# Kernel optimization log

Measured on AMD Instinct MI355X. Metric: run time of the kernel, lower is better.

The kernel has to match this reference:

```python
import jax, jax.numpy as jnp
import numpy as np

B, S, E, H = 4, 1024, 256, 8
D = E // H


def setup_inputs() -> dict:
    key = jax.random.key(0)
    ks = jax.random.split(key, 10)
    def lin(k, fin, fout):
        return jax.random.normal(k, (fin, fout), jnp.float32) / np.sqrt(fin)
    return {
        'x': jax.random.normal(ks[0], (B, S, E), jnp.float32),
        'Wq': lin(ks[1], E, E),
        'Wk': lin(ks[2], E, E),
        'Wv': lin(ks[3], E, E),
        'W_off1': lin(ks[4], E, E // 2),
        'b_off1': jnp.zeros((E // 2,), jnp.float32),
        'W_off2': lin(ks[5], E // 2, 2 * H),
        'b_off2': jnp.zeros((2 * H,), jnp.float32),
        'W_out': lin(ks[6], E, E),
        'b_out': jnp.zeros((E,), jnp.float32),
    }


def _forward(x, Wq, Wk, Wv, W_off1, b_off1, W_off2, b_off2, W_out, b_out):
    Bb, Ss, Ee = x.shape
    scale = 1.0 / np.sqrt(D)
    # offsets: (B,S,H,2) -- [...,0]=x-offset (col), [...,1]=y-offset (row)
    off = jax.nn.gelu(x @ W_off1 + b_off1, approximate=False) @ W_off2 + b_off2
    off = off.reshape(Bb, Ss, H, 2)
    q = (x @ Wq).reshape(Bb, Ss, H, D).transpose(0, 2, 1, 3)  # bhsd
    k = (x @ Wk).reshape(Bb, Ss, H, D).transpose(0, 2, 1, 3)
    v = (x @ Wv).reshape(Bb, Ss, H, D).transpose(0, 2, 1, 3)
    scores = jnp.einsum('bhid,bhjd->bhij', q, k) * scale  # (B,H,S,S)

    ox = off[..., 0].transpose(0, 2, 1)  # (B,H,S)
    oy = off[..., 1].transpose(0, 2, 1)
    cols = jnp.arange(Ss, dtype=x.dtype)
    xs = cols[None, None, None, :] + ox[..., None]          # (B,H,S,S) sample col
    ys = cols[None, None, :, None] + oy[..., None]          # (B,H,S,1) sample row

    x0 = jnp.floor(xs); x1 = x0 + 1.0
    y0 = jnp.floor(ys); y1 = y0 + 1.0
    wx = xs - x0  # (B,H,S,S)
    wy = ys - y0  # (B,H,S,1)
    lim = jnp.asarray(Ss - 1, x.dtype)

    def corner(yf, xf):
        # bilinear corner sample with zeros padding (align_corners=True)
        yc = jnp.clip(yf, 0, lim).astype(jnp.int32)
        xc = jnp.clip(xf, 0, lim).astype(jnp.int32)
        rows = jnp.take_along_axis(scores, jnp.broadcast_to(yc, scores.shape), axis=2)
        vals = jnp.take_along_axis(rows, jnp.broadcast_to(xc, rows.shape), axis=3)
        valid = (yf >= 0) & (yf <= lim) & (xf >= 0) & (xf <= lim)
        return jnp.where(valid, vals, jnp.zeros((), x.dtype))

    deformed = (corner(y0, x0) * (1 - wy) * (1 - wx)
                + corner(y0, x1) * (1 - wy) * wx
                + corner(y1, x0) * wy * (1 - wx)
                + corner(y1, x1) * wy * wx)

    attn = jax.nn.softmax(deformed, axis=-1)  # dropout is identity in eval
    out = jnp.einsum('bhij,bhjd->bhid', attn, v)
    out = out.transpose(0, 2, 1, 3).reshape(Bb, Ss, Ee)
    return out @ W_out + b_out


def reference(x, Wq, Wk, Wv, W_off1, b_off1, W_off2, b_off2, W_out, b_out):
    return _forward(x, Wq, Wk, Wv, W_off1, b_off1, W_off2, b_off2, W_out, b_out)
```

## Files before the change

kernel.cpp:

```cpp
#include <hip/hip_runtime.h>

typedef unsigned short u16;
typedef __attribute__((ext_vector_type(8))) unsigned short ushort8_t;
typedef __attribute__((ext_vector_type(8))) short short8;
typedef __attribute__((ext_vector_type(4))) float f32x4;

__device__ __forceinline__ float bf2f(u16 u) {
    union { unsigned int i; float f; } z;
    z.i = ((unsigned int)u) << 16;
    return z.f;
}
__device__ __forceinline__ u16 f2bf(float f) {
    union { float f; unsigned int i; } z;
    z.f = f;
    unsigned int i = z.i;
    return (u16)((i + 0x7fffu + ((i >> 16) & 1u)) >> 16);
}
__device__ __forceinline__ int sniff_bf16(const u16* __restrict__ x) {
    u16 u = x[threadIdx.x & 63];
    int e = (u >> 7) & 0xFF;
    bool sane = (e >= 110 && e <= 135) || (u == 0);
    unsigned long long m = __ballot(sane);
    return (__popcll(m) >= 50) ? 1 : 0;
}
__device__ __forceinline__ float cvt_elem(const void* p, int i, int fl) {
    return fl ? bf2f(((const u16*)p)[i]) : ((const float*)p)[i];
}

#define SB 1024
#define EB 256
#define NH 8
#define HD 32

__global__ __launch_bounds__(256) void k_convx(
    const void* x, const void* w2, const void* b1, const void* b2, const void* bo,
    u16* __restrict__ xb, u16* __restrict__ W2t, float* __restrict__ b1f,
    float* __restrict__ b2f, float* __restrict__ bof) {
    int fl = sniff_bf16((const u16*)x);
    int t = threadIdx.x;
    if (blockIdx.x < 1024) {
        int idx = blockIdx.x * 1024 + t * 4;
        if (fl) {
            *(ushort4*)(xb + idx) = *(const ushort4*)((const u16*)x + idx);
        } else {
            float4 v = *(const float4*)((const float*)x + idx);
            ushort4 s;
            s.x = f2bf(v.x); s.y = f2bf(v.y); s.z = f2bf(v.z); s.w = f2bf(v.w);
            *(ushort4*)(xb + idx) = s;
        }
    } else {
        #pragma unroll
        for (int it = 0; it < 10; ++it) {
            int idx = it * 256 + t;
            if (idx < 2048) {
                int n = idx >> 7, kk = idx & 127;
                W2t[idx] = f2bf(cvt_elem(w2, kk * 16 + n, fl));
            }
            else if (idx < 2176)  b1f[idx - 2048] = cvt_elem(b1, idx - 2048, fl);
            else if (idx < 2192)  b2f[idx - 2176] = cvt_elem(b2, idx - 2176, fl);
            else if (idx < 2448)  bof[idx - 2192] = cvt_elem(bo, idx - 2192, fl);
        }
    }
}

__global__ __launch_bounds__(256) void k_trans(
    const void* wq, const void* wk, const void* wv, const void* w1, const void* wo,
    const u16* __restrict__ xsniff, u16* __restrict__ Wcat, u16* __restrict__ Wot) {
    __shared__ float tile[64][65];
    int fl = sniff_bf16(xsniff);
    int z = blockIdx.z;
    const void* src;
    u16* dst;
    int ncols;
    if (z == 0)      { src = wq; dst = Wcat;             ncols = 256; }
    else if (z == 1) { src = wk; dst = Wcat + 256 * 256; ncols = 256; }
    else if (z == 2) { src = wv; dst = Wcat + 512 * 256; ncols = 256; }
    else if (z == 3) { src = w1; dst = Wcat + 768 * 256; ncols = 128; }
    else             { src = wo; dst = Wot;              ncols = 256; }
    int k0 = blockIdx.x * 64, n0 = blockIdx.y * 64;
    if (n0 >= ncols) return;
    int t = threadIdx.x;
    int lr = t >> 6, lc = t & 63;
    #pragma unroll
    for (int it = 0; it < 16; ++it) {
        int r = it * 4 + lr;
        tile[r][lc] = cvt_elem(src, (k0 + r) * ncols + n0 + lc, fl);
    }
    __syncthreads();
    #pragma unroll
    for (int it = 0; it < 16; ++it) {
        int n = it * 4 + lr;
        dst[(size_t)(n0 + n) * 256 + k0 + lc] = f2bf(tile[lc][n]);
    }
}

__global__ __launch_bounds__(256) void k_qkvh(
    const u16* __restrict__ xb, const u16* __restrict__ Wt, const float* __restrict__ b1f,
    u16* __restrict__ q, u16* __restrict__ k, u16* __restrict__ v, u16* __restrict__ hb) {
    int t = threadIdx.x;
    int w = t >> 6, L = t & 63;
    int lane15 = L & 15, quad = L >> 4;
    int Wid = blockIdx.x * 4 + w;
    int mtile = Wid & 127, ntile = Wid >> 7;
    int m0 = mtile * 32, n0 = ntile * 32;
    const u16* ap0 = xb + (size_t)(m0 + lane15) * 256 + quad * 8;
    const u16* ap1 = ap0 + 16 * 256;
    const u16* bp0 = Wt + (size_t)(n0 + lane15) * 256 + quad * 8;
    const u16* bp1 = bp0 + 16 * 256;
    f32x4 acc[2][2];
    #pragma unroll
    for (int a = 0; a < 2; ++a)
        #pragma unroll
        for (int c = 0; c < 2; ++c) acc[a][c] = (f32x4){0.0f, 0.0f, 0.0f, 0.0f};
    #pragma unroll
    for (int kc = 0; kc < 256; kc += 32) {
        short8 a0 = *(const short8*)(ap0 + kc);
        short8 a1 = *(const short8*)(ap1 + kc);
        short8 b0 = *(const short8*)(bp0 + kc);
        short8 b1 = *(const short8*)(bp1 + kc);
        acc[0][0] = __builtin_amdgcn_mfma_f32_16x16x32_bf16(a0, b0, acc[0][0], 0, 0, 0);
        acc[0][1] = __builtin_amdgcn_mfma_f32_16x16x32_bf16(a0, b1, acc[0][1], 0, 0, 0);
        acc[1][0] = __builtin_amdgcn_mfma_f32_16x16x32_bf16(a1, b0, acc[1][0], 0, 0, 0);
        acc[1][1] = __builtin_amdgcn_mfma_f32_16x16x32_bf16(a1, b1, acc[1][1], 0, 0, 0);
    }
    if (ntile < 16) {
        u16* dst = (ntile < 8) ? q : k;
        int nl = (ntile & 7) * 32;
        #pragma unroll
        for (int mt = 0; mt < 2; ++mt)
            #pragma unroll
            for (int nt = 0; nt < 2; ++nt)
                #pragma unroll
                for (int reg = 0; reg < 4; ++reg) {
                    int m = m0 + mt * 16 + quad * 4 + reg;
                    int n = nl + nt * 16 + lane15;
                    int b = m >> 10, s = m & 1023, hh = n >> 5, d = n & 31;
                    dst[(((size_t)(b * NH + hh)) * SB + s) * HD + d] = f2bf(acc[mt][nt][reg]);
                }
    } else if (ntile < 24) {
        int nl = (ntile - 16) * 32;
        #pragma unroll
        for (int mt = 0; mt < 2; ++mt)
            #pragma unroll
            for (int nt = 0; nt < 2; ++nt)
                #pragma unroll
                for (int reg = 0; reg < 4; ++reg) {
                    int m = m0 + mt * 16 + quad * 4 + reg;
                    int n = nl + nt * 16 + lane15;
                    int b = m >> 10, s = m & 1023, hh = n >> 5, d = n & 31;
                    v[(b * NH + hh) * (SB * HD) + (s >> 3) * 256 + d * 8 + (s & 7)] =
                        f2bf(acc[mt][nt][reg]);
                }
    } else {
        int nl = (ntile - 24) * 32;
        #pragma unroll
        for (int mt = 0; mt < 2; ++mt)
            #pragma unroll
            for (int nt = 0; nt < 2; ++nt)
                #pragma unroll
                for (int reg = 0; reg < 4; ++reg) {
                    int m = m0 + mt * 16 + quad * 4 + reg;
                    int hn = nl + nt * 16 + lane15;
                    float aa = acc[mt][nt][reg] + b1f[hn];
                    float g = 0.5f * aa * (1.0f + erff(aa * 0.70710678118654752f));
                    hb[(size_t)m * 128 + hn] = f2bf(g);
                }
    }
}

__global__ __launch_bounds__(256) void k_qprime(
    const u16* __restrict__ hb, const u16* __restrict__ W2t, const float* __restrict__ b2f,
    float2* __restrict__ prmA, float4* __restrict__ prmB) {
    int t = threadIdx.x;
    int w = t >> 6, L = t & 63;
    int lane15 = L & 15, quad = L >> 4;
    int m0 = (blockIdx.x * 4 + w) * 16;
    const u16* ap = hb + (size_t)(m0 + lane15) * 128 + quad * 8;
    const u16* bp = W2t + (size_t)lane15 * 128 + quad * 8;
    f32x4 acc = {0.0f, 0.0f, 0.0f, 0.0f};
    #pragma unroll
    for (int c = 0; c < 4; ++c) {
        short8 a = *(const short8*)(ap + c * 32);
        short8 bfr = *(const short8*)(bp + c * 32);
        acc = __builtin_amdgcn_mfma_f32_16x16x32_bf16(a, bfr, acc, 0, 0, 0);
    }
    const float scale = 0.17677669529663687f;
    int n = lane15, h = n >> 1;
    float bb = b2f[n];
    #pragma unroll
    for (int reg = 0; reg < 4; ++reg) {
        int m = m0 + quad * 4 + reg;
        int i = m & 1023;
        float val = acc[reg] + bb;
        if ((n & 1) == 0) {
            float fxf = floorf(val);
            float wx = val - fxf;
            fxf = fminf(fmaxf(fxf, -1028.0f), 1028.0f);
            prmA[m * 8 + h] = make_float2(fxf, wx);
        } else {
            float ysf = (float)i + val;
            float y0f = floorf(ysf);
            float wy = ysf - y0f;
            float y1f = y0f + 1.0f;
            float alA = scale * (1.0f - wy) * ((y0f >= 0.0f && y0f <= 1023.0f) ? 1.0f : 0.0f);
            float alB = scale * wy * ((y1f >= 0.0f && y1f <= 1023.0f) ? 1.0f : 0.0f);
            float yc0 = fminf(fmaxf(y0f, 0.0f), 1023.0f);
            float yc1 = fminf(fmaxf(y1f, 0.0f), 1023.0f);
            prmB[m * 8 + h] = make_float4(alA, alB, yc0, yc1);
        }
    }
}

#define TSTR 1064
#define BLEND4A(R)                                                    \
    _Pragma("unroll")                                                 \
    for (int jj = 0; jj < 4; ++jj) {                                  \
        float dd = wxm * A8[(R) + jj] + wx * A8[(R) + jj + 1];        \
        dv[c * 4 + jj] = dd;                                          \
        lmax = fmaxf(lmax, dd);                                       \
    }

__global__ __launch_bounds__(256) void k_attn(
    const u16* __restrict__ q, const u16* __restrict__ kmat,
    const float2* __restrict__ prmA, const float4* __restrict__ prmB,
    const u16* __restrict__ vfrag, u16* __restrict__ attn) {
    __shared__ u16 tbuf[16][TSTR];
    __shared__ float invLs[16];
    float* red = (float*)&tbuf[0][0];
    int t = threadIdx.x;
    int w = t >> 6, L = t & 63;
    int lane15 = L & 15, quad = L >> 4;
    int bh = blockIdx.y, it0 = blockIdx.x * 16;
    int b = bh >> 3, h = bh & 7;
    int mg0 = b * SB + it0;

    const u16* qb = q + (size_t)bh * SB * HD;
    float4 pB = prmB[(size_t)(mg0 + lane15) * 8 + h];
    int yc0 = (int)pB.z, yc1 = (int)pB.w;
    short8 q0 = *(const short8*)(qb + yc0 * HD + quad * 8);
    short8 q1 = *(const short8*)(qb + yc1 * HD + quad * 8);
    union { short8 v; u16 a[8]; } afr;
    #pragma unroll
    for (int s = 0; s < 8; ++s)
        afr.a[s] = f2bf(pB.x * bf2f((u16)q0[s]) + pB.y * bf2f((u16)q1[s]));

    const u16* kb = kmat + (size_t)bh * SB * HD;
    int c0 = w * 256;
    #pragma unroll
    for (int nt = 0; nt < 16; ++nt) {
        short8 bk = *(const short8*)(kb + (size_t)(c0 + nt * 16 + lane15) * HD + quad * 8);
        f32x4 z = {0.0f, 0.0f, 0.0f, 0.0f};
        f32x4 acc = __builtin_amdgcn_mfma_f32_16x16x32_bf16(afr.v, bk, z, 0, 0, 0);
        #pragma unroll
        for (int reg = 0; reg < 4; ++reg)
            tbuf[quad * 4 + reg][16 + c0 + nt * 16 + lane15] = f2bf(acc[reg]);
    }
    __syncthreads();

    #pragma unroll
    for (int r = 0; r < 4; ++r) {
        int m = w * 4 + r;
        float2 pA = prmA[(size_t)(mg0 + m) * 8 + h];
        int fx = (int)pA.x;
        float wx = pA.y, wxm = 1.0f - wx;
        int qd = fx >> 2, rm = fx & 3;
        float dv[16];
        float lmax = -3.0e38f;
        #pragma unroll
        for (int c = 0; c < 4; ++c) {
            int colbase = c * 256 + 4 * (qd + L);
            int rd = colbase < -16 ? -16 : (colbase > 1032 ? 1032 : colbase);
            const u16* rp = &tbuf[m][16 + rd];
            ushort4 lo = *(const ushort4*)rp;
            ushort4 hi = *(const ushort4*)(rp + 4);
            u16 av[8] = {lo.x, lo.y, lo.z, lo.w, hi.x, hi.y, hi.z, hi.w};
            float A8[8];
            #pragma unroll
            for (int s = 0; s < 8; ++s) {
                bool ok = (unsigned)(colbase + s) < 1024u;
                A8[s] = ok ? bf2f(av[s]) : 0.0f;
            }
            if (rm == 0) { BLEND4A(0) }
            else if (rm == 1) { BLEND4A(1) }
            else if (rm == 2) { BLEND4A(2) }
            else { BLEND4A(3) }
        }
        #pragma unroll
        for (int o = 1; o < 64; o <<= 1) lmax = fmaxf(lmax, __shfl_xor(lmax, o));
        float ls = 0.0f;
        #pragma unroll
        for (int z = 0; z < 16; ++z) { dv[z] = __expf(dv[z] - lmax); ls += dv[z]; }
        #pragma unroll
        for (int o = 1; o < 64; o <<= 1) ls += __shfl_xor(ls, o);
        #pragma unroll
        for (int c = 0; c < 4; ++c) {
            unsigned lo = (unsigned)f2bf(dv[c * 4 + 0]) | ((unsigned)f2bf(dv[c * 4 + 1]) << 16);
            unsigned hi = (unsigned)f2bf(dv[c * 4 + 2]) | ((unsigned)f2bf(dv[c * 4 + 3]) << 16);
            *(uint2*)&tbuf[m][16 + c * 256 + 4 * L] = make_uint2(lo, hi);
        }
        if (L == 0) invLs[m] = 1.0f / ls;
    }
    __syncthreads();

    const u16* vb = vfrag + bh * (SB * HD);
    f32x4 acc0 = {0.0f, 0.0f, 0.0f, 0.0f};
    f32x4 acc1 = {0.0f, 0.0f, 0.0f, 0.0f};
    int kc0 = w * 256;
    #pragma unroll
    for (int c = 0; c < 8; ++c) {
        int kc = kc0 + c * 32;
        short8 a = *(const short8*)&tbuf[lane15][16 + kc + quad * 8];
        const u16* bp = vb + ((kc >> 3) + quad) * (HD * 8);
        short8 b0 = *(const short8*)(bp + lane15 * 8);
        short8 b1 = *(const short8*)(bp + (lane15 + 16) * 8);
        acc0 = __builtin_amdgcn_mfma_f32_16x16x32_bf16(a, b0, acc0, 0, 0, 0);
        acc1 = __builtin_amdgcn_mfma_f32_16x16x32_bf16(a, b1, acc1, 0, 0, 0);
    }
    __syncthreads();
    *(f32x4*)&red[(((size_t)w * 2 + 0) * 64 + L) * 4] = acc0;
    *(f32x4*)&red[(((size_t)w * 2 + 1) * 64 + L) * 4] = acc1;
    __syncthreads();
    {
        int row = t >> 4, col = t & 15;
        int lsrc = col + 16 * (row >> 2);
        int reg = row & 3;
        float s0 = red[((0 * 64 + lsrc)) * 4 + reg] + red[((2 * 64 + lsrc)) * 4 + reg]
                 + red[((4 * 64 + lsrc)) * 4 + reg] + red[((6 * 64 + lsrc)) * 4 + reg];
        float s1 = red[((1 * 64 + lsrc)) * 4 + reg] + red[((3 * 64 + lsrc)) * 4 + reg]
                 + red[((5 * 64 + lsrc)) * 4 + reg] + red[((7 * 64 + lsrc)) * 4 + reg];
        float il = invLs[row];
        size_t o = ((size_t)(b * SB + it0 + row)) * EB + h * HD;
        attn[o + col]      = f2bf(s0 * il);
        attn[o + 16 + col] = f2bf(s1 * il);
    }
}

__global__ __launch_bounds__(256) void k_out(
    const u16* __restrict__ a, const u16* __restrict__ Wot, const float* __restrict__ bof,
    const u16* __restrict__ xsniff, void* __restrict__ outp) {
    int fl = sniff_bf16(xsniff);
    int t = threadIdx.x;
    int w = t >> 6, L = t & 63;
    int lane15 = L & 15, quad = L >> 4;
    int Wid = blockIdx.x * 4 + w;
    int m0 = (Wid & 255) * 16, n0 = (Wid >> 8) * 32;
    const u16* ap  = a + (size_t)(m0 + lane15) * 256 + quad * 8;
    const u16* bp0 = Wot + (size_t)(n0 + lane15) * 256 + quad * 8;
    const u16* bp1 = bp0 + 16 * 256;
    f32x4 acc0 = {0.0f, 0.0f, 0.0f, 0.0f};
    f32x4 acc1 = {0.0f, 0.0f, 0.0f, 0.0f};
    #pragma unroll
    for (int kc = 0; kc < 256; kc += 32) {
        short8 av = *(const short8*)(ap + kc);
        short8 b0 = *(const short8*)(bp0 + kc);
        short8 b1 = *(const short8*)(bp1 + kc);
        acc0 = __builtin_amdgcn_mfma_f32_16x16x32_bf16(av, b0, acc0, 0, 0, 0);
        acc1 = __builtin_amdgcn_mfma_f32_16x16x32_bf16(av, b1, acc1, 0, 0, 0);
    }
    #pragma unroll
    for (int nt = 0; nt < 2; ++nt) {
        const f32x4& ac = nt ? acc1 : acc0;
        #pragma unroll
        for (int reg = 0; reg < 4; ++reg) {
            int m = m0 + quad * 4 + reg;
            int n = n0 + nt * 16 + lane15;
            float val = ac[reg] + bof[n];
            if (fl) ((u16*)outp)[(size_t)m * 256 + n] = f2bf(val);
            else    ((float*)outp)[(size_t)m * 256 + n] = val;
        }
    }
}

extern "C" void kernel_launch(void* const* d_in, const int* in_sizes, int n_in,
                              void* d_out, int out_size, void* d_ws, size_t ws_size,
                              hipStream_t stream) {
    char* ws = (char*)d_ws;
    u16*    xb   = (u16*)(ws);
    u16*    Wcat = (u16*)(ws + 2097152);
    u16*    Wot  = (u16*)(ws + 2555904);
    u16*    W2t  = (u16*)(ws + 2686976);
    float*  b1f  = (float*)(ws + 2691072);
    float*  b2f  = (float*)(ws + 2691584);
    float*  bof  = (float*)(ws + 2691648);
    u16*    q    = (u16*)(ws + 2692672);
    u16*    k    = (u16*)(ws + 4789824);
    u16*    v    = (u16*)(ws + 6886976);
    u16*    hb   = (u16*)(ws + 8984128);
    u16*    attn = (u16*)(ws + 10032704);
    float2* prmA = (float2*)(ws + 12129856);
    float4* prmB = (float4*)(ws + 12392000);

    hipLaunchKernelGGL(k_convx, dim3(1025), dim3(256), 0, stream,
                       d_in[0], d_in[6], d_in[5], d_in[7], d_in[9],
                       xb, W2t, b1f, b2f, bof);
    hipLaunchKernelGGL(k_trans, dim3(4, 4, 5), dim3(256), 0, stream,
                       d_in[1], d_in[2], d_in[3], d_in[4], d_in[8],
                       (const u16*)d_in[0], Wcat, Wot);
    hipLaunchKernelGGL(k_qkvh, dim3(896), dim3(256), 0, stream, xb, Wcat, b1f, q, k, v, hb);
    hipLaunchKernelGGL(k_qprime, dim3(64), dim3(256), 0, stream, hb, W2t, b2f, prmA, prmB);
    hipLaunchKernelGGL(k_attn, dim3(64, 32), dim3(256), 0, stream, q, k, prmA, prmB, v, attn);
    hipLaunchKernelGGL(k_out, dim3(512), dim3(256), 0, stream, attn, Wot, bof,
                       (const u16*)d_in[0], (u16*)d_out);
}
```

Before: 149.9 us.

## Merge prep kernels, swap MFMA operands for vectorized stores, zero-pad score tile

Merges the input-conversion and weight-transpose kernels into one launch, which removes a kernel launch. Swaps the MFMA A/B operands in the QKV, attention-score and output GEMMs so each lane holds four contiguous output columns and can issue packed 64-bit or float4 stores instead of scalar ones. Zero-fills the padding columns of the shared score tile, so the per-element bounds masks in the bilinear blend can be dropped, and shrinks the row stride. The stride change may bring back LDS bank conflicts, and correctness now depends on the padding being wide enough.

```diff
diff --git a/kernel.cpp b/kernel.cpp
--- a/kernel.cpp
+++ b/kernel.cpp
@@ -1,7 +1,6 @@
 #include <hip/hip_runtime.h>
 
 typedef unsigned short u16;
-typedef __attribute__((ext_vector_type(8))) unsigned short ushort8_t;
 typedef __attribute__((ext_vector_type(8))) short short8;
 typedef __attribute__((ext_vector_type(4))) float f32x4;
 
@@ -32,14 +31,18 @@
 #define NH 8
 #define HD 32
 
-__global__ __launch_bounds__(256) void k_convx(
-    const void* x, const void* w2, const void* b1, const void* b2, const void* bo,
-    u16* __restrict__ xb, u16* __restrict__ W2t, float* __restrict__ b1f,
-    float* __restrict__ b2f, float* __restrict__ bof) {
+__global__ __launch_bounds__(256) void k_prep(
+    const void* x, const void* wq, const void* wk, const void* wv, const void* w1,
+    const void* w2, const void* wo, const void* b1, const void* b2, const void* bo,
+    u16* __restrict__ xb, u16* __restrict__ Wcat, u16* __restrict__ Wot,
+    u16* __restrict__ W2t, float* __restrict__ b1f, float* __restrict__ b2f,
+    float* __restrict__ bof) {
+    __shared__ float tile[64][65];
     int fl = sniff_bf16((const u16*)x);
     int t = threadIdx.x;
-    if (blockIdx.x < 1024) {
-        int idx = blockIdx.x * 1024 + t * 4;
+    int bid = blockIdx.x;
+    if (bid < 1024) {
+        int idx = bid * 1024 + t * 4;
         if (fl) {
             *(ushort4*)(xb + idx) = *(const ushort4*)((const u16*)x + idx);
         } else {
@@ -48,7 +51,7 @@
             s.x = f2bf(v.x); s.y = f2bf(v.y); s.z = f2bf(v.z); s.w = f2bf(v.w);
             *(ushort4*)(xb + idx) = s;
         }
-    } else {
+    } else if (bid == 1024) {
         #pragma unroll
         for (int it = 0; it < 10; ++it) {
             int idx = it * 256 + t;
@@ -60,37 +63,31 @@
             else if (idx < 2192)  b2f[idx - 2176] = cvt_elem(b2, idx - 2176, fl);
             else if (idx < 2448)  bof[idx - 2192] = cvt_elem(bo, idx - 2192, fl);
         }
-    }
-}
-
-__global__ __launch_bounds__(256) void k_trans(
-    const void* wq, const void* wk, const void* wv, const void* w1, const void* wo,
-    const u16* __restrict__ xsniff, u16* __restrict__ Wcat, u16* __restrict__ Wot) {
-    __shared__ float tile[64][65];
-    int fl = sniff_bf16(xsniff);
-    int z = blockIdx.z;
-    const void* src;
-    u16* dst;
-    int ncols;
-    if (z == 0)      { src = wq; dst = Wcat;             ncols = 256; }
-    else if (z == 1) { src = wk; dst = Wcat + 256 * 256; ncols = 256; }
-    else if (z == 2) { src = wv; dst = Wcat + 512 * 256; ncols = 256; }
-    else if (z == 3) { src = w1; dst = Wcat + 768 * 256; ncols = 128; }
-    else             { src = wo; dst = Wot;              ncols = 256; }
-    int k0 = blockIdx.x * 64, n0 = blockIdx.y * 64;
-    if (n0 >= ncols) return;
-    int t = threadIdx.x;
-    int lr = t >> 6, lc = t & 63;
-    #pragma unroll
-    for (int it = 0; it < 16; ++it) {
-        int r = it * 4 + lr;
-        tile[r][lc] = cvt_elem(src, (k0 + r) * ncols + n0 + lc, fl);
-    }
-    __syncthreads();
-    #pragma unroll
-    for (int it = 0; it < 16; ++it) {
-        int n = it * 4 + lr;
-        dst[(size_t)(n0 + n) * 256 + k0 + lc] = f2bf(tile[lc][n]);
+    } else {
+        int rel = bid - 1025;
+        int z = rel >> 4, rr = rel & 15;
+        int k0 = (rr & 3) * 64, n0 = (rr >> 2) * 64;
+        const void* src;
+        u16* dst;
+        int ncols;
+        if (z == 0)      { src = wq; dst = Wcat;             ncols = 256; }
+        else if (z == 1) { src = wk; dst = Wcat + 256 * 256; ncols = 256; }
+        else if (z == 2) { src = wv; dst = Wcat + 512 * 256; ncols = 256; }
+        else if (z == 3) { src = w1; dst = Wcat + 768 * 256; ncols = 128; }
+        else             { src = wo; dst = Wot;              ncols = 256; }
+        if (n0 >= ncols) return;
+        int lr = t >> 6, lc = t & 63;
+        #pragma unroll
+        for (int it = 0; it < 16; ++it) {
+            int r = it * 4 + lr;
+            tile[r][lc] = cvt_elem(src, (k0 + r) * ncols + n0 + lc, fl);
+        }
+        __syncthreads();
+        #pragma unroll
+        for (int it = 0; it < 16; ++it) {
+            int n = it * 4 + lr;
+            dst[(size_t)(n0 + n) * 256 + k0 + lc] = f2bf(tile[lc][n]);
+        }
     }
 }
 
@@ -107,64 +104,84 @@
     const u16* ap1 = ap0 + 16 * 256;
     const u16* bp0 = Wt + (size_t)(n0 + lane15) * 256 + quad * 8;
     const u16* bp1 = bp0 + 16 * 256;
+    bool vreg = (ntile >= 16 && ntile < 24);
     f32x4 acc[2][2];
     #pragma unroll
     for (int a = 0; a < 2; ++a)
         #pragma unroll
         for (int c = 0; c < 2; ++c) acc[a][c] = (f32x4){0.0f, 0.0f, 0.0f, 0.0f};
-    #pragma unroll
-    for (int kc = 0; kc < 256; kc += 32) {
-        short8 a0 = *(const short8*)(ap0 + kc);
-        short8 a1 = *(const short8*)(ap1 + kc);
-        short8 b0 = *(const short8*)(bp0 + kc);
-        short8 b1 = *(const short8*)(bp1 + kc);
-        acc[0][0] = __builtin_amdgcn_mfma_f32_16x16x32_bf16(a0, b0, acc[0][0], 0, 0, 0);
-        acc[0][1] = __builtin_amdgcn_mfma_f32_16x16x32_bf16(a0, b1, acc[0][1], 0, 0, 0);
-        acc[1][0] = __builtin_amdgcn_mfma_f32_16x16x32_bf16(a1, b0, acc[1][0], 0, 0, 0);
-        acc[1][1] = __builtin_amdgcn_mfma_f32_16x16x32_bf16(a1, b1, acc[1][1], 0, 0, 0);
+    if (!vreg) {
+        #pragma unroll
+        for (int kc = 0; kc < 256; kc += 32) {
+            short8 a0 = *(const short8*)(ap0 + kc);
+            short8 a1 = *(const short8*)(ap1 + kc);
+            short8 b0 = *(const short8*)(bp0 + kc);
+            short8 b1 = *(const short8*)(bp1 + kc);
+            acc[0][0] = __builtin_amdgcn_mfma_f32_16x16x32_bf16(b0, a0, acc[0][0], 0, 0, 0);
+            acc[0][1] = __builtin_amdgcn_mfma_f32_16x16x32_bf16(b1, a0, acc[0][1], 0, 0, 0);
+            acc[1][0] = __builtin_amdgcn_mfma_f32_16x16x32_bf16(b0, a1, acc[1][0], 0, 0, 0);
+            acc[1][1] = __builtin_amdgcn_mfma_f32_16x16x32_bf16(b1, a1, acc[1][1], 0, 0, 0);
+        }
+    } else {
+        #pragma unroll
+        for (int kc = 0; kc < 256; kc += 32) {
+            short8 a0 = *(const short8*)(ap0 + kc);
+            short8 a1 = *(const short8*)(ap1 + kc);
+            short8 b0 = *(const short8*)(bp0 + kc);
+            short8 b1 = *(const short8*)(bp1 + kc);
+            acc[0][0] = __builtin_amdgcn_mfma_f32_16x16x32_bf16(a0, b0, acc[0][0], 0, 0, 0);
+            acc[0][1] = __builtin_amdgcn_mfma_f32_16x16x32_bf16(a0, b1, acc[0][1], 0, 0, 0);
+            acc[1][0] = __builtin_amdgcn_mfma_f32_16x16x32_bf16(a1, b0, acc[1][0], 0, 0, 0);
+            acc[1][1] = __builtin_amdgcn_mfma_f32_16x16x32_bf16(a1, b1, acc[1][1], 0, 0, 0);
+        }
     }
     if (ntile < 16) {
         u16* dst = (ntile < 8) ? q : k;
-        int nl = (ntile & 7) * 32;
+        int hh = ntile & 7;
+        #pragma unroll
+        for (int xt = 0; xt < 2; ++xt)
+            #pragma unroll
+            for (int wt = 0; wt < 2; ++wt) {
+                int m = m0 + xt * 16 + lane15;
+                int b = m >> 10, s = m & 1023;
+                int d = wt * 16 + quad * 4;
+                ushort4 st;
+                st.x = f2bf(acc[xt][wt][0]); st.y = f2bf(acc[xt][wt][1]);
+                st.z = f2bf(acc[xt][wt][2]); st.w = f2bf(acc[xt][wt][3]);
+                *(ushort4*)(dst + (((size_t)(b * NH + hh)) * SB + s) * HD + d) = st;
+            }
+    } else if (vreg) {
+        int nl = (ntile - 16) * 32;
         #pragma unroll
         for (int mt = 0; mt < 2; ++mt)
             #pragma unroll
-            for (int nt = 0; nt < 2; ++nt)
+            for (int nt = 0; nt < 2; ++nt) {
+                int n = nl + nt * 16 + lane15;
+                int hh = n >> 5, d = n & 31;
+                int mbase = m0 + mt * 16 + quad * 4;
+                int b = mbase >> 10, s0 = mbase & 1023;
+                ushort4 st;
+                st.x = f2bf(acc[mt][nt][0]); st.y = f2bf(acc[mt][nt][1]);
+                st.z = f2bf(acc[mt][nt][2]); st.w = f2bf(acc[mt][nt][3]);
+                *(ushort4*)(v + (b * NH + hh) * (SB * HD) + (s0 >> 3) * 256 + d * 8 + (s0 & 7)) = st;
+            }
+    } else {
+        int nl = (ntile - 24) * 32;
+        #pragma unroll
+        for (int xt = 0; xt < 2; ++xt)
+            #pragma unroll
+            for (int wt = 0; wt < 2; ++wt) {
+                int m = m0 + xt * 16 + lane15;
+                int hn = nl + wt * 16 + quad * 4;
+                ushort4 st;
                 #pragma unroll
                 for (int reg = 0; reg < 4; ++reg) {
-                    int m = m0 + mt * 16 + quad * 4 + reg;
-                    int n = nl + nt * 16 + lane15;
-                    int b = m >> 10, s = m & 1023, hh = n >> 5, d = n & 31;
-                    dst[(((size_t)(b * NH + hh)) * SB + s) * HD + d] = f2bf(acc[mt][nt][reg]);
+                    float aa = acc[xt][wt][reg] + b1f[hn + reg];
+                    float g = 0.5f * aa * (1.0f + erff(aa * 0.70710678118654752f));
+                    ((u16*)&st)[reg] = f2bf(g);
                 }
-    } else if (ntile < 24) {
-        int nl = (ntile - 16) * 32;
-        #pragma unroll
-        for (int mt = 0; mt < 2; ++mt)
-            #pragma unroll
-            for (int nt = 0; nt < 2; ++nt)
-                #pragma unroll
-                for (int reg = 0; reg < 4; ++reg) {
-                    int m = m0 + mt * 16 + quad * 4 + reg;
-                    int n = nl + nt * 16 + lane15;
-                    int b = m >> 10, s = m & 1023, hh = n >> 5, d = n & 31;
-                    v[(b * NH + hh) * (SB * HD) + (s >> 3) * 256 + d * 8 + (s & 7)] =
-                        f2bf(acc[mt][nt][reg]);
-                }
-    } else {
-        int nl = (ntile - 24) * 32;
-        #pragma unroll
-        for (int mt = 0; mt < 2; ++mt)
-            #pragma unroll
-            for (int nt = 0; nt < 2; ++nt)
-                #pragma unroll
-                for (int reg = 0; reg < 4; ++reg) {
-                    int m = m0 + mt * 16 + quad * 4 + reg;
-                    int hn = nl + nt * 16 + lane15;
-                    float aa = acc[mt][nt][reg] + b1f[hn];
-                    float g = 0.5f * aa * (1.0f + erff(aa * 0.70710678118654752f));
-                    hb[(size_t)m * 128 + hn] = f2bf(g);
-                }
+                *(ushort4*)(hb + (size_t)m * 128 + hn) = st;
+            }
     }
 }
 
@@ -211,7 +228,7 @@
     }
 }
 
-#define TSTR 1064
+#define TSTR 1056
 #define BLEND4A(R)                                                    \
     _Pragma("unroll")                                                 \
     for (int jj = 0; jj < 4; ++jj) {                                  \
@@ -234,6 +251,12 @@
     int b = bh >> 3, h = bh & 7;
     int mg0 = b * SB + it0;
 
+    {
+        int row = t >> 4, ii = t & 15;
+        tbuf[row][ii] = 0;
+        tbuf[row][1040 + ii] = 0;
+    }
+
     const u16* qb = q + (size_t)bh * SB * HD;
     float4 pB = prmB[(size_t)(mg0 + lane15) * 8 + h];
     int yc0 = (int)pB.z, yc1 = (int)pB.w;
@@ -250,10 +273,11 @@
     for (int nt = 0; nt < 16; ++nt) {
         short8 bk = *(const short8*)(kb + (size_t)(c0 + nt * 16 + lane15) * HD + quad * 8);
         f32x4 z = {0.0f, 0.0f, 0.0f, 0.0f};
-        f32x4 acc = __builtin_amdgcn_mfma_f32_16x16x32_bf16(afr.v, bk, z, 0, 0, 0);
-        #pragma unroll
-        for (int reg = 0; reg < 4; ++reg)
-            tbuf[quad * 4 + reg][16 + c0 + nt * 16 + lane15] = f2bf(acc[reg]);
+        f32x4 acc = __builtin_amdgcn_mfma_f32_16x16x32_bf16(bk, afr.v, z, 0, 0, 0);
+        uint2 pk;
+        pk.x = (unsigned)f2bf(acc[0]) | ((unsigned)f2bf(acc[1]) << 16);
+        pk.y = (unsigned)f2bf(acc[2]) | ((unsigned)f2bf(acc[3]) << 16);
+        *(uint2*)&tbuf[lane15][16 + c0 + nt * 16 + quad * 4] = pk;
     }
     __syncthreads();
 
@@ -273,13 +297,9 @@
             const u16* rp = &tbuf[m][16 + rd];
             ushort4 lo = *(const ushort4*)rp;
             ushort4 hi = *(const ushort4*)(rp + 4);
-            u16 av[8] = {lo.x, lo.y, lo.z, lo.w, hi.x, hi.y, hi.z, hi.w};
             float A8[8];
-            #pragma unroll
-            for (int s = 0; s < 8; ++s) {
-                bool ok = (unsigned)(colbase + s) < 1024u;
-                A8[s] = ok ? bf2f(av[s]) : 0.0f;
-            }
+            A8[0] = bf2f(lo.x); A8[1] = bf2f(lo.y); A8[2] = bf2f(lo.z); A8[3] = bf2f(lo.w);
+            A8[4] = bf2f(hi.x); A8[5] = bf2f(hi.y); A8[6] = bf2f(hi.z); A8[7] = bf2f(hi.w);
             if (rm == 0) { BLEND4A(0) }
             else if (rm == 1) { BLEND4A(1) }
             else if (rm == 2) { BLEND4A(2) }
@@ -354,19 +374,22 @@
         short8 av = *(const short8*)(ap + kc);
         short8 b0 = *(const short8*)(bp0 + kc);
         short8 b1 = *(const short8*)(bp1 + kc);
-        acc0 = __builtin_amdgcn_mfma_f32_16x16x32_bf16(av, b0, acc0, 0, 0, 0);
-        acc1 = __builtin_amdgcn_mfma_f32_16x16x32_bf16(av, b1, acc1, 0, 0, 0);
-    }
-    #pragma unroll
-    for (int nt = 0; nt < 2; ++nt) {
-        const f32x4& ac = nt ? acc1 : acc0;
-        #pragma unroll
-        for (int reg = 0; reg < 4; ++reg) {
-            int m = m0 + quad * 4 + reg;
-            int n = n0 + nt * 16 + lane15;
-            float val = ac[reg] + bof[n];
-            if (fl) ((u16*)outp)[(size_t)m * 256 + n] = f2bf(val);
-            else    ((float*)outp)[(size_t)m * 256 + n] = val;
+        acc0 = __builtin_amdgcn_mfma_f32_16x16x32_bf16(b0, av, acc0, 0, 0, 0);
+        acc1 = __builtin_amdgcn_mfma_f32_16x16x32_bf16(b1, av, acc1, 0, 0, 0);
+    }
+    int m = m0 + lane15;
+    #pragma unroll
+    for (int wt = 0; wt < 2; ++wt) {
+        const f32x4& ac = wt ? acc1 : acc0;
+        int n = n0 + wt * 16 + quad * 4;
+        float4 bz = *(const float4*)(bof + n);
+        float v0 = ac[0] + bz.x, v1 = ac[1] + bz.y, v2 = ac[2] + bz.z, v3 = ac[3] + bz.w;
+        if (fl) {
+            ushort4 st;
+            st.x = f2bf(v0); st.y = f2bf(v1); st.z = f2bf(v2); st.w = f2bf(v3);
+            *(ushort4*)((u16*)outp + (size_t)m * 256 + n) = st;
+        } else {
+            *(float4*)((float*)outp + (size_t)m * 256 + n) = make_float4(v0, v1, v2, v3);
         }
     }
 }
@@ -390,12 +413,10 @@
     float2* prmA = (float2*)(ws + 12129856);
     float4* prmB = (float4*)(ws + 12392000);
 
-    hipLaunchKernelGGL(k_convx, dim3(1025), dim3(256), 0, stream,
-                       d_in[0], d_in[6], d_in[5], d_in[7], d_in[9],
-                       xb, W2t, b1f, b2f, bof);
-    hipLaunchKernelGGL(k_trans, dim3(4, 4, 5), dim3(256), 0, stream,
-                       d_in[1], d_in[2], d_in[3], d_in[4], d_in[8],
-                       (const u16*)d_in[0], Wcat, Wot);
+    hipLaunchKernelGGL(k_prep, dim3(1105), dim3(256), 0, stream,
+                       d_in[0], d_in[1], d_in[2], d_in[3], d_in[4],
+                       d_in[6], d_in[8], d_in[5], d_in[7], d_in[9],
+                       xb, Wcat, Wot, W2t, b1f, b2f, bof);
     hipLaunchKernelGGL(k_qkvh, dim3(896), dim3(256), 0, stream, xb, Wcat, b1f, q, k, v, hb);
     hipLaunchKernelGGL(k_qprime, dim3(64), dim3(256), 0, stream, hb, W2t, b2f, prmA, prmB);
     hipLaunchKernelGGL(k_attn, dim3(64, 32), dim3(256), 0, stream, q, k, prmA, prmB, v, attn);
```

Measured after the change: 147.9 us. Within noise of the previous version (-1.3%).
